# Performance work log

Hardware: AMD Instinct MI355X
Metric: run time of the kernel (lower is better)

The kernel has to match this reference:

```python
import jax, jax.numpy as jnp
import numpy as np
from jax import lax

B, T, E, H, A, V = 128, 64, 512, 512, 512, 10000


def setup_inputs() -> dict:
    key = jax.random.key(0)
    ks = jax.random.split(key, 16)
    # lengths: descending, in [1, T], first forced to T (pack_padded_sequence requirement)
    ln = np.asarray(jax.random.randint(ks[0], (B,), 1, T + 1))
    ln = np.sort(ln)[::-1].copy()
    ln[0] = T
    u = lambda k, s, a=0.1: jax.random.uniform(k, s, jnp.float32, -a, a)
    return {
        "features": jax.random.normal(ks[1], (B, E), jnp.float32),
        "captions": jax.random.randint(ks[2], (B, T - 1), 0, V),
        "lengths": jnp.asarray(ln, jnp.int64) if jax.config.jax_enable_x64 else jnp.asarray(ln, jnp.int32),
        "cnn_features": jax.random.normal(ks[3], (B, A), jnp.float32),
        "emb_W": u(ks[4], (V, E)),
        "W_ih": u(ks[5], (4 * H, E), 1.0 / np.sqrt(H)),
        "W_hh": u(ks[6], (4 * H, H), 1.0 / np.sqrt(H)),
        "b_ih": u(ks[7], (4 * H,), 1.0 / np.sqrt(H)),
        "b_hh": u(ks[8], (4 * H,), 1.0 / np.sqrt(H)),
        "att_W": u(ks[9], (A, H + E)),
        "att_b": jnp.zeros((A,), jnp.float32),
        "attd_W": u(ks[10], (E, A + E)),
        "attd_b": jnp.zeros((E,), jnp.float32),
        "out_W": u(ks[11], (V, H)),
        "out_b": jnp.zeros((V,), jnp.float32),
    }


def _lstm_cell(x, h, c, W_ih, W_hh, b_ih, b_hh):
    g = x @ W_ih.T + b_ih + h @ W_hh.T + b_hh  # (B, 4H)
    i, f, gg, o = jnp.split(g, 4, axis=-1)
    i = jax.nn.sigmoid(i); f = jax.nn.sigmoid(f)
    gg = jnp.tanh(gg); o = jax.nn.sigmoid(o)
    c2 = f * c + i * gg
    return o * jnp.tanh(c2), c2


def reference(features, captions, lengths, cnn_features, emb_W, W_ih, W_hh, b_ih, b_hh,
              att_W, att_b, attd_W, attd_b, out_W, out_b):
    emb = emb_W[captions]                                    # (B, T-1, E)
    xs = jnp.concatenate([features[:, None, :], emb], 1)     # (B, T, E)
    h0 = jnp.zeros((B, H), xs.dtype)
    c0 = jnp.zeros((B, H), xs.dtype)
    # step 0: plain LSTM on raw input, zero initial state (all sequences active)
    h1, c1 = _lstm_cell(xs[:, 0], h0, c0, W_ih, W_hh, b_ih, b_hh)

    def step(carry, inp):
        h, c = carry
        x, t = inp                                           # x: (B, E)
        aw = jax.nn.softmax(jnp.concatenate([x, h], 1) @ att_W.T + att_b, axis=1)
        attended = cnn_features * aw                         # (B, A)
        x2 = jnp.concatenate([x, attended], 1) @ attd_W.T + attd_b  # (B, E)
        h2, c2 = _lstm_cell(x2, h, c, W_ih, W_hh, b_ih, b_hh)
        active = (t < lengths)[:, None]
        h = jnp.where(active, h2, h)
        c = jnp.where(active, c2, c)
        return (h, c), jnp.where(active, h2, jnp.zeros_like(h2))

    xs_t = jnp.swapaxes(xs[:, 1:], 0, 1)                     # (T-1, B, E)
    _, outs = lax.scan(step, (h1, c1), (xs_t, jnp.arange(1, T)))
    hidden = jnp.concatenate([h1[None], outs], 0)            # (T, B, H)
    logits = hidden @ out_W.T + out_b                        # (T, B, V)
    valid = (jnp.arange(T)[:, None] < lengths[None, :])      # (T, B)
    return jnp.where(valid[:, :, None], logits, jnp.zeros_like(logits))
```

## Files before the change

kernel.cpp:

```cpp
#include <hip/hip_runtime.h>
#include <hip/hip_bf16.h>

#define B 128
#define T 64
#define E 512
#define H 512
#define AA 512
#define V 10000

typedef __hip_bfloat16 bf16;
typedef unsigned long long u64;
typedef unsigned short u16;
typedef __attribute__((ext_vector_type(8))) short bf16x8s;
typedef __attribute__((ext_vector_type(4))) float f32x4;

#define MFMA __builtin_amdgcn_mfma_f32_16x16x32_bf16

__device__ __forceinline__ bf16x8s ld8(const bf16* p) {
  return *reinterpret_cast<const bf16x8s*>(p);
}
__device__ __forceinline__ float sigm(float x) { return 1.f / (1.f + __expf(-x)); }
__device__ __forceinline__ float bf2f(u16 u) {
  return __uint_as_float(((unsigned)u) << 16);
}


__global__ __launch_bounds__(256) void kxs(const float* __restrict__ feat,
                                           const int* __restrict__ cap,
                                           const float* __restrict__ embW,
                                           bf16* __restrict__ xs) {
  int idx = blockIdx.x * 256 + threadIdx.x;
  int e4 = (idx & 127) << 2;
  int b = (idx >> 7) & 127;
  int t = idx >> 14;
  const float* src = (t == 0) ? (feat + (size_t)b * E)
                              : (embW + (size_t)cap[b * (T - 1) + (t - 1)] * E);
  float4 v = *reinterpret_cast<const float4*>(src + e4);
  bf16* d = xs + ((size_t)t * B + b) * E + e4;
  d[0] = __float2bfloat16(v.x); d[1] = __float2bfloat16(v.y);
  d[2] = __float2bfloat16(v.z); d[3] = __float2bfloat16(v.w);
}

__global__ __launch_bounds__(256) void kcast(const float* __restrict__ s,
                                             bf16* __restrict__ d, int n4) {
  int i = blockIdx.x * 256 + threadIdx.x;
  if (i >= n4) return;
  float4 v = *reinterpret_cast<const float4*>(s + (size_t)i * 4);
  d[i * 4 + 0] = __float2bfloat16(v.x); d[i * 4 + 1] = __float2bfloat16(v.y);
  d[i * 4 + 2] = __float2bfloat16(v.z); d[i * 4 + 3] = __float2bfloat16(v.w);
}

__global__ __launch_bounds__(256) void kslice(const float* __restrict__ src,
                                              bf16* __restrict__ dst, int c0) {
  int i = blockIdx.x * 256 + threadIdx.x;
  int row = i >> 7, c4 = (i & 127) << 2;
  float4 v = *reinterpret_cast<const float4*>(src + (size_t)row * 1024 + c0 + c4);
  bf16* d = dst + (size_t)row * 512 + c4;
  d[0] = __float2bfloat16(v.x); d[1] = __float2bfloat16(v.y);
  d[2] = __float2bfloat16(v.z); d[3] = __float2bfloat16(v.w);
}

__global__ __launch_bounds__(256) void ktrans(const float* __restrict__ src,
                                              bf16* __restrict__ dst, int coff) {
  __shared__ float tl[32][33];
  int bx = blockIdx.x & 15, by = blockIdx.x >> 4;
  int tx = threadIdx.x & 31, ty = threadIdx.x >> 5;
  for (int yy = ty; yy < 32; yy += 8)
    tl[yy][tx] = src[(size_t)(by * 32 + yy) * 1024 + coff + bx * 32 + tx];
  __syncthreads();
  for (int yy = ty; yy < 32; yy += 8)
    dst[(size_t)(bx * 32 + yy) * 512 + by * 32 + tx] = __float2bfloat16(tl[tx][yy]);
}

__global__ __launch_bounds__(256) void kpadW(const float* __restrict__ s,
                                             bf16* __restrict__ d) {
  int i = blockIdx.x * 256 + threadIdx.x;
  int row = (i << 2) / H;
  float4 v = make_float4(0.f, 0.f, 0.f, 0.f);
  if (row < V) v = *reinterpret_cast<const float4*>(s + (size_t)i * 4);
  d[i * 4 + 0] = __float2bfloat16(v.x); d[i * 4 + 1] = __float2bfloat16(v.y);
  d[i * 4 + 2] = __float2bfloat16(v.z); d[i * 4 + 3] = __float2bfloat16(v.w);
}

__global__ __launch_bounds__(256) void kgb(const float* __restrict__ bih,
                                           const float* __restrict__ bhh,
                                           const float* __restrict__ Wih_f,
                                           const float* __restrict__ attdb,
                                           float* __restrict__ gb0,
                                           float* __restrict__ gbA) {
  int g = blockIdx.x * 256 + threadIdx.x;
  if (g >= 2048) return;
  float b0 = bih[g] + bhh[g];
  float s = 0.f;
  for (int e = 0; e < 512; ++e) s += Wih_f[(size_t)g * 512 + e] * attdb[e];
  gb0[g] = b0; gbA[g] = b0 + s;
}

__global__ __launch_bounds__(256) void kgemm(const bf16* __restrict__ Ag,
                                             const bf16* __restrict__ Bg,
                                             const float* __restrict__ bias,
                                             bf16* __restrict__ outB,
                                             int nbn, int Nld) {
  __shared__ __align__(16) char lds[2][2][16384];
  const int nwg = gridDim.x;
  const int bid0 = blockIdx.x;
  const int wg = (bid0 & 7) * (nwg >> 3) + (bid0 >> 3);
  const int bm = wg / nbn, bn = wg % nbn;
  const int tid = threadIdx.x, w = tid >> 6, lane = tid & 63;
  const int fr = lane & 15, fq = lane >> 4, ko = fq << 3;
  const int mh = w >> 1, nh = w & 1;
  const bf16* Abase = Ag + (size_t)bm * 128 * 512;
  const bf16* Bbase = Bg + (size_t)bn * 128 * 512;
  f32x4 acc[4][4] = {};
  auto STAGE = [&](int buf, int k0) {
    #pragma unroll
    for (int m = 0; m < 2; ++m) {
      const bf16* base = m ? Bbase : Abase;
      #pragma unroll
      for (int it = 0; it < 4; ++it) {
        int si = tid + it * 256;
        int row = si >> 3;
        int s = (si & 7) ^ (row & 7);
        __builtin_amdgcn_global_load_lds(
          (const __attribute__((address_space(1))) void*)(base + (size_t)row * 512 + k0 + s * 8),
          (__attribute__((address_space(3))) void*)(&lds[buf][m][((tid & ~63) + it * 256) * 16]),
          16, 0, 0);
      }
    }
  };
  STAGE(0, 0);
  __syncthreads();
  for (int kt = 0; kt < 8; ++kt) {
    int cur = kt & 1;
    if (kt < 7) STAGE(cur ^ 1, (kt + 1) * 64);
    #pragma unroll
    for (int kk = 0; kk < 64; kk += 32) {
      bf16x8s a[4], b[4];
      #pragma unroll
      for (int i = 0; i < 4; ++i) {
        int ra = mh * 64 + i * 16 + fr;
        a[i] = *reinterpret_cast<const bf16x8s*>(
            &lds[cur][0][ra * 128 + ((((kk + ko) >> 3) ^ (ra & 7)) << 4)]);
        int rb = nh * 64 + i * 16 + fr;
        b[i] = *reinterpret_cast<const bf16x8s*>(
            &lds[cur][1][rb * 128 + ((((kk + ko) >> 3) ^ (rb & 7)) << 4)]);
      }
      #pragma unroll
      for (int mi = 0; mi < 4; ++mi)
        #pragma unroll
        for (int ni = 0; ni < 4; ++ni)
          acc[mi][ni] = MFMA(a[mi], b[ni], acc[mi][ni], 0, 0, 0);
    }
    __syncthreads();
  }
  #pragma unroll
  for (int mi = 0; mi < 4; ++mi)
    #pragma unroll
    for (int ni = 0; ni < 4; ++ni)
      #pragma unroll
      for (int j = 0; j < 4; ++j) {
        int row = bm * 128 + mh * 64 + mi * 16 + fq * 4 + j;
        int col = bn * 128 + nh * 64 + ni * 16 + fr;
        float bv = bias ? bias[col] : 0.f;
        outB[(size_t)row * Nld + col] = __float2bfloat16(acc[mi][ni][j] + bv);
      }
}

__global__ __launch_bounds__(256, 4) void kfinal(const bf16* __restrict__ Ag,
                                                 const bf16* __restrict__ Bg,
                                                 const float* __restrict__ bias,
                                                 const int* __restrict__ len,
                                                 float* __restrict__ out) {
  __shared__ __align__(16) char lds[2][2][8192];
  const int nwg = gridDim.x;
  const int bid0 = blockIdx.x;
  const int wg = (bid0 & 7) * (nwg >> 3) + (bid0 >> 3);
  const int bm = wg / 79, bn = wg % 79;
  const int tid = threadIdx.x, w = tid >> 6, lane = tid & 63;
  const int fr = lane & 15, fq = lane >> 4;
  const int mh = w >> 1, nh = w & 1;
  const bf16* Abase = Ag + (size_t)bm * 128 * 512;
  const bf16* Bbase = Bg + (size_t)bn * 128 * 512;
  f32x4 acc[4][4] = {};
  auto STAGE = [&](int buf, int k0) {
    #pragma unroll
    for (int m = 0; m < 2; ++m) {
      const bf16* base = m ? Bbase : Abase;
      #pragma unroll
      for (int it = 0; it < 2; ++it) {
        int u = it * 256 + tid;
        int row = u >> 2, c = u & 3;
        int cs = c ^ ((row >> 1) & 3);
        __builtin_amdgcn_global_load_lds(
          (const __attribute__((address_space(1))) void*)(base + (size_t)row * 512 + k0 + cs * 8),
          (__attribute__((address_space(3))) void*)(&lds[buf][m][((tid & ~63) + it * 256) * 16]),
          16, 0, 0);
      }
    }
  };
  STAGE(0, 0);
  __syncthreads();
  for (int kt = 0; kt < 16; ++kt) {
    int cur = kt & 1;
    if (kt < 15) STAGE(cur ^ 1, (kt + 1) * 32);
    bf16x8s a[4], b[4];
    #pragma unroll
    for (int i = 0; i < 4; ++i) {
      int ra = mh * 64 + i * 16 + fr;
      a[i] = *reinterpret_cast<const bf16x8s*>(
          &lds[cur][0][ra * 64 + ((fq ^ ((ra >> 1) & 3)) << 4)]);
      int rb = nh * 64 + i * 16 + fr;
      b[i] = *reinterpret_cast<const bf16x8s*>(
          &lds[cur][1][rb * 64 + ((fq ^ ((rb >> 1) & 3)) << 4)]);
    }
    #pragma unroll
    for (int mi = 0; mi < 4; ++mi)
      #pragma unroll
      for (int ni = 0; ni < 4; ++ni)
        acc[mi][ni] = MFMA(a[mi], b[ni], acc[mi][ni], 0, 0, 0);
    __syncthreads();
  }
  #pragma unroll
  for (int mi = 0; mi < 4; ++mi)
    #pragma unroll
    for (int ni = 0; ni < 4; ++ni)
      #pragma unroll
      for (int j = 0; j < 4; ++j) {
        int row = bm * 128 + mh * 64 + mi * 16 + fq * 4 + j;
        int col = bn * 128 + nh * 64 + ni * 16 + fr;
        if (col < V) {
          int tt = row >> 7, bb = row & 127;
          out[(size_t)row * V + col] = (tt < len[bb]) ? acc[mi][ni][j] + bias[col] : 0.f;
        }
      }
}

__global__ __launch_bounds__(512, 1) void kloop(
    const bf16* __restrict__ Sxb,
    const bf16* __restrict__ Gx,
    const bf16* __restrict__ Kc,
    const bf16* __restrict__ Whh,
    const bf16* __restrict__ WaH,
    const float* __restrict__ gb0,
    const float* __restrict__ gbA,
    const float* __restrict__ cnn,
    const int* __restrict__ len,
    bf16* __restrict__ hstore,
    bf16* __restrict__ pstore,
    float* __restrict__ Zbuf,
    bf16* __restrict__ hid,
    int* ticket, int* winner, int* flags) {
  __shared__ __align__(16) char KcS[65536];
  __shared__ __align__(16) char WhS[65536];
  __shared__ int steam[2];

  if (threadIdx.x == 0) {
    int xcc;
    asm volatile("s_getreg_b32 %0, hwreg(HW_REG_XCC_ID)" : "=s"(xcc));
    xcc &= 15;
    int my = __hip_atomic_fetch_add(&ticket[xcc], 1, __ATOMIC_RELAXED,
                                    __HIP_MEMORY_SCOPE_AGENT);
    if (my == 31) {
      int exp = -1;
      __hip_atomic_compare_exchange_strong(winner, &exp, xcc, __ATOMIC_RELAXED,
                                           __ATOMIC_RELAXED, __HIP_MEMORY_SCOPE_AGENT);
    }
    int wv;
    while ((wv = __hip_atomic_load(winner, __ATOMIC_RELAXED,
                                   __HIP_MEMORY_SCOPE_AGENT)) < 0)
      __builtin_amdgcn_s_sleep(8);
    steam[0] = (wv == xcc && my < 32) ? 1 : 0;
    steam[1] = my;
  }
  __syncthreads();
  if (!steam[0]) return;
  const int wid = steam[1];

  const int tid = threadIdx.x, w = tid >> 6, lane = tid & 63;
  const int fr = lane & 15, fq = lane >> 4, ko = fq << 3;
  const int cb = wid << 4;
  const int col = cb + fr;

  for (int u = tid; u < 4096; u += 512) {
    int row = u >> 6, chunk = u & 63;
    int g = (row >> 4) * 512 + cb + (row & 15);
    int off = row * 1024 + ((chunk ^ (row & 7)) << 4);
    *reinterpret_cast<bf16x8s*>(&KcS[off]) = ld8(Kc + (size_t)g * 512 + chunk * 8);
    *reinterpret_cast<bf16x8s*>(&WhS[off]) = ld8(Whh + (size_t)g * 512 + chunk * 8);
  }

  const int r0 = w * 16 + fq * 4;
  int4 lv4 = *reinterpret_cast<const int4*>(len + r0);
  int lv[4] = {lv4.x, lv4.y, lv4.z, lv4.w};
  float cnnv[4], gb0v[4], gbAv[4];
  #pragma unroll
  for (int j = 0; j < 4; ++j) cnnv[j] = cnn[(size_t)(r0 + j) * AA + col];
  #pragma unroll
  for (int q = 0; q < 4; ++q) {
    gb0v[q] = gb0[q * 512 + col];
    gbAv[q] = gbA[q * 512 + col];
  }
  float cstv[4] = {0.f, 0.f, 0.f, 0.f};
  u16 hpv[4] = {0, 0, 0, 0};
  __syncthreads();

  auto arrive = [&](int ep2) {
    __syncthreads();
    if (tid == 0)
      __hip_atomic_store(flags + wid * 16, ep2, __ATOMIC_RELAXED,
                         __HIP_MEMORY_SCOPE_AGENT);
  };
  auto wait = [&](int ep2) {
    if (tid < 64) {
      const int* fp = flags + (tid & 31) * 16;
      while (__ballot(__hip_atomic_load(fp, __ATOMIC_RELAXED,
                                        __HIP_MEMORY_SCOPE_AGENT) < ep2))
        __builtin_amdgcn_s_sleep(1);
    }
    __syncthreads();
  };

  int ep = 0;
  for (int t = 0; t < T; ++t) {
    if (t) { ++ep; arrive(ep); }
    u16 gxv[16];
    u16 sxv[4] = {0, 0, 0, 0};
    #pragma unroll
    for (int q = 0; q < 4; ++q)
      #pragma unroll
      for (int j = 0; j < 4; ++j)
        gxv[q * 4 + j] = __builtin_nontemporal_load(
            (const u16*)Gx + ((size_t)t * B + r0 + j) * 2048 + q * 512 + col);
    if (t) {
      #pragma unroll
      for (int j = 0; j < 4; ++j)
        sxv[j] = __builtin_nontemporal_load(
            (const u16*)Sxb + ((size_t)t * B + r0 + j) * AA + col);
    }
    const bf16* hin = hstore + (size_t)(t ? t - 1 : 0) * B * H;
    bf16* pst = pstore + (size_t)t * B * AA;
    if (t) {
      wait(ep);
      f32x4 acc1 = {};
      {
        const bf16* ha = hin + (size_t)(w * 16 + fr) * H + ko;
        const bf16* wb = WaH + (size_t)col * H + ko;
        #pragma unroll 4
        for (int k = 0; k < 512; k += 32)
          acc1 = MFMA(ld8(ha + k), ld8(wb + k), acc1, 0, 0, 0);
      }
      float pj[4];
      #pragma unroll
      for (int j = 0; j < 4; ++j) {
        pj[j] = __expf(acc1[j] + bf2f(sxv[j]));
        bf16 pb = __float2bfloat16(pj[j] * cnnv[j]);
        pst[(size_t)(r0 + j) * AA + col] = pb;
      }
      #pragma unroll
      for (int j = 0; j < 4; ++j) {
        float z = pj[j];
        z += __shfl_xor(z, 1); z += __shfl_xor(z, 2);
        z += __shfl_xor(z, 4); z += __shfl_xor(z, 8);
        if (fr == 0)
          __hip_atomic_fetch_add(Zbuf + t * B + r0 + j, z, __ATOMIC_RELAXED,
                                 __HIP_MEMORY_SCOPE_WORKGROUP);
      }
      ++ep; arrive(ep);
    }
    f32x4 accH[4] = {}, accP[4] = {};
    if (t) {
      {
        const bf16* ha = hin + (size_t)(w * 16 + fr) * H + ko;
        #pragma unroll 2
        for (int k = 0; k < 512; k += 32) {
          bf16x8s a = ld8(ha + k);
          #pragma unroll
          for (int q = 0; q < 4; ++q) {
            bf16x8s b = *reinterpret_cast<const bf16x8s*>(
                &WhS[(q * 16 + fr) * 1024 + ((((k >> 3) + fq) ^ (fr & 7)) << 4)]);
            accH[q] = MFMA(a, b, accH[q], 0, 0, 0);
          }
        }
      }
      wait(ep);
      {
        const bf16* pa = pst + (size_t)(w * 16 + fr) * AA + ko;
        #pragma unroll 2
        for (int k = 0; k < 512; k += 32) {
          bf16x8s a = ld8(pa + k);
          #pragma unroll
          for (int q = 0; q < 4; ++q) {
            bf16x8s b = *reinterpret_cast<const bf16x8s*>(
                &KcS[(q * 16 + fr) * 1024 + ((((k >> 3) + fq) ^ (fr & 7)) << 4)]);
            accP[q] = MFMA(a, b, accP[q], 0, 0, 0);
          }
        }
      }
      float4 zv = *reinterpret_cast<const float4*>(Zbuf + t * B + r0);
      float zp[4] = {zv.x, zv.y, zv.z, zv.w};
      #pragma unroll
      for (int q = 0; q < 4; ++q)
        #pragma unroll
        for (int j = 0; j < 4; ++j)
          accP[q][j] *= __fdividef(1.f, zp[j]);
    }
    float gsel[4];
    #pragma unroll
    for (int q = 0; q < 4; ++q) gsel[q] = t ? gbAv[q] : gb0v[q];
    #pragma unroll
    for (int j = 0; j < 4; ++j) {
      float gi = sigm(accP[0][j] + accH[0][j] + gsel[0] + bf2f(gxv[0 + j]));
      float gf = sigm(accP[1][j] + accH[1][j] + gsel[1] + bf2f(gxv[4 + j]));
      float gg = tanhf(accP[2][j] + accH[2][j] + gsel[2] + bf2f(gxv[8 + j]));
      float go = sigm(accP[3][j] + accH[3][j] + gsel[3] + bf2f(gxv[12 + j]));
      float c2 = gf * cstv[j] + gi * gg;
      float h2 = go * tanhf(c2);
      bool act = t < lv[j];
      if (act) cstv[j] = c2;
      bf16 hb = __float2bfloat16(h2);
      u16 hbits = *reinterpret_cast<u16*>(&hb);
      hpv[j] = act ? hbits : hpv[j];
      ((u16*)hstore)[((size_t)t * B + r0 + j) * H + col] = hpv[j];
      __builtin_nontemporal_store(act ? hbits : (u16)0,
          (u16*)hid + ((size_t)t * B + r0 + j) * H + col);
    }
  }
}


extern "C" void kernel_launch(void* const* d_in, const int* in_sizes, int n_in,
                              void* d_out, int out_size, void* d_ws, size_t ws_size,
                              hipStream_t stream) {
  const float* feat   = (const float*)d_in[0];
  const int*   cap    = (const int*)d_in[1];
  const int*   len    = (const int*)d_in[2];
  const float* cnn    = (const float*)d_in[3];
  const float* embW   = (const float*)d_in[4];
  const float* Wih_f  = (const float*)d_in[5];
  const float* Whh_f  = (const float*)d_in[6];
  const float* bih    = (const float*)d_in[7];
  const float* bhh    = (const float*)d_in[8];
  const float* attW_f = (const float*)d_in[9];
  const float* attb   = (const float*)d_in[10];
  const float* attdW_f= (const float*)d_in[11];
  const float* attdb  = (const float*)d_in[12];
  const float* outW_f = (const float*)d_in[13];
  const float* outb   = (const float*)d_in[14];
  float* out = (float*)d_out;
  char* ws = (char*)d_ws;

  size_t off = 0;
  auto alloc = [&](size_t n) { char* p = ws + off; off += (n + 255) & ~(size_t)255; return p; };
  bf16*  xs    = (bf16*)alloc(8388608);
  bf16*  WaX   = (bf16*)alloc(524288);
  bf16*  WaH   = (bf16*)alloc(524288);
  bf16*  WdXT  = (bf16*)alloc(524288);
  bf16*  WdAT  = (bf16*)alloc(524288);
  bf16*  Wihb  = (bf16*)alloc(2097152);
  bf16*  Whhb  = (bf16*)alloc(2097152);
  bf16*  Kc    = (bf16*)alloc(2097152);
  bf16*  outWp = (bf16*)alloc(10354688);
  bf16*  Sxb   = (bf16*)alloc(8388608);
  bf16*  Gx    = (bf16*)alloc(33554432);
  bf16*  hid   = (bf16*)alloc(8388608);
  bf16*  hstore= (bf16*)alloc(8388608);
  bf16*  pstore= (bf16*)alloc(8388608);
  float* gb0   = (float*)alloc(8192);
  float* gbA   = (float*)alloc(8192);
  float* Zbuf  = (float*)alloc(32768);
  int*   ticket= (int*)alloc(256);
  int*   winner= (int*)alloc(256);
  int*   flags = (int*)alloc(2048);
  bf16*  Kx    = pstore;

  kxs<<<4096, 256, 0, stream>>>(feat, cap, embW, xs);
  kslice<<<256, 256, 0, stream>>>(attW_f, WaX, 0);
  kslice<<<256, 256, 0, stream>>>(attW_f, WaH, 512);
  ktrans<<<256, 256, 0, stream>>>(attdW_f, WdXT, 0);
  ktrans<<<256, 256, 0, stream>>>(attdW_f, WdAT, 512);
  kcast<<<1024, 256, 0, stream>>>(Wih_f, Wihb, 262144);
  kcast<<<1024, 256, 0, stream>>>(Whh_f, Whhb, 262144);
  kpadW<<<5056, 256, 0, stream>>>(outW_f, outWp);
  kgb<<<8, 256, 0, stream>>>(bih, bhh, Wih_f, attdb, gb0, gbA);

  kgemm<<<256, 256, 0, stream>>>(xs, WaX, attb, Sxb, 4, 512);
  kgemm<<<64, 256, 0, stream>>>(Wihb, WdXT, nullptr, Kx, 4, 512);
  kgemm<<<64, 256, 0, stream>>>(Wihb, WdAT, nullptr, Kc, 4, 512);
  kgemm<<<1024, 256, 0, stream>>>(xs, Kx, nullptr, Gx, 16, 2048);
  kgemm<<<16, 256, 0, stream>>>(xs, Wihb, nullptr, Gx, 16, 2048);

  hipMemsetAsync(ticket, 0, 256, stream);
  hipMemsetAsync(winner, 0xFF, 256, stream);
  hipMemsetAsync(flags, 0, 2048, stream);
  hipMemsetAsync(Zbuf, 0, 32768, stream);

  kloop<<<256, 512, 0, stream>>>(Sxb, Gx, Kc, Whhb, WaH, gb0, gbA, cnn, len,
                                 hstore, pstore, Zbuf, hid, ticket, winner, flags);

  kfinal<<<5056, 256, 0, stream>>>(hid, outWp, outb, len, out);
}
```

Measured before the change: 1.706 ms.

## Prepack per-thread Gx/Sx inputs, stage WaH in LDS, reuse h fragments

A new kpack kernel rearranges the precomputed input-gate and attention-score tensors so each thread of the recurrent loop fetches its 16+4 values with a few contiguous 64-bit loads instead of scattered 2-byte loads. The recurrent kernel also caches its WaH slice in shared memory and loads the previous hidden state fragments once into registers, reusing them for both the attention and recurrent MFMAs. The goal is to shorten the serial per-step latency of the persistent loop, at the cost of an extra pass over about 40 MB and more register pressure.

Result: slower. 1.780 ms (+4.3%).

```diff
diff --git a/kernel.cpp b/kernel.cpp
--- a/kernel.cpp
+++ b/kernel.cpp
@@ -94,6 +94,33 @@
   float s = 0.f;
   for (int e = 0; e < 512; ++e) s += Wih_f[(size_t)g * 512 + e] * attdb[e];
   gb0[g] = b0; gbA[g] = b0 + s;
+}
+
+__global__ __launch_bounds__(512) void kpack(const u16* __restrict__ Gx,
+                                             const u16* __restrict__ Sxb,
+                                             u16* __restrict__ Gxp,
+                                             u16* __restrict__ Sxp) {
+  int bid = blockIdx.x;
+  int t = bid >> 5, wid = bid & 31;
+  int tid = threadIdx.x;
+  int w = tid >> 6, lane = tid & 63;
+  int fr = lane & 15, fq = lane >> 4;
+  int r0 = w * 16 + fq * 4;
+  int cb = wid << 4;
+  u16 g[16], s[4];
+  #pragma unroll
+  for (int q = 0; q < 4; ++q)
+    #pragma unroll
+    for (int j = 0; j < 4; ++j)
+      g[q * 4 + j] = Gx[((size_t)t * B + r0 + j) * 2048 + q * 512 + cb + fr];
+  #pragma unroll
+  for (int j = 0; j < 4; ++j)
+    s[j] = Sxb[((size_t)t * B + r0 + j) * AA + cb + fr];
+  size_t ob = ((size_t)bid * 512 + tid);
+  #pragma unroll
+  for (int k = 0; k < 16; ++k) Gxp[ob * 16 + k] = g[k];
+  #pragma unroll
+  for (int j = 0; j < 4; ++j) Sxp[ob * 4 + j] = s[j];
 }
 
 __global__ __launch_bounds__(256) void kgemm(const bf16* __restrict__ Ag,
@@ -236,8 +263,8 @@
 }
 
 __global__ __launch_bounds__(512, 1) void kloop(
-    const bf16* __restrict__ Sxb,
-    const bf16* __restrict__ Gx,
+    const u16* __restrict__ Sxp,
+    const u16* __restrict__ Gxp,
     const bf16* __restrict__ Kc,
     const bf16* __restrict__ Whh,
     const bf16* __restrict__ WaH,
@@ -252,6 +279,7 @@
     int* ticket, int* winner, int* flags) {
   __shared__ __align__(16) char KcS[65536];
   __shared__ __align__(16) char WhS[65536];
+  __shared__ __align__(16) char WaS[16384];
   __shared__ int steam[2];
 
   if (threadIdx.x == 0) {
@@ -287,6 +315,11 @@
     int off = row * 1024 + ((chunk ^ (row & 7)) << 4);
     *reinterpret_cast<bf16x8s*>(&KcS[off]) = ld8(Kc + (size_t)g * 512 + chunk * 8);
     *reinterpret_cast<bf16x8s*>(&WhS[off]) = ld8(Whh + (size_t)g * 512 + chunk * 8);
+  }
+  for (int u = tid; u < 1024; u += 512) {
+    int row = u >> 6, chunk = u & 63;
+    *reinterpret_cast<bf16x8s*>(&WaS[row * 1024 + ((chunk ^ (row & 7)) << 4)]) =
+        ld8(WaH + (size_t)(cb + row) * 512 + chunk * 8);
   }
 
   const int r0 = w * 16 + fq * 4;
@@ -323,38 +356,37 @@
   int ep = 0;
   for (int t = 0; t < T; ++t) {
     if (t) { ++ep; arrive(ep); }
-    u16 gxv[16];
-    u16 sxv[4] = {0, 0, 0, 0};
-    #pragma unroll
-    for (int q = 0; q < 4; ++q)
-      #pragma unroll
-      for (int j = 0; j < 4; ++j)
-        gxv[q * 4 + j] = __builtin_nontemporal_load(
-            (const u16*)Gx + ((size_t)t * B + r0 + j) * 2048 + q * 512 + col);
-    if (t) {
-      #pragma unroll
-      for (int j = 0; j < 4; ++j)
-        sxv[j] = __builtin_nontemporal_load(
-            (const u16*)Sxb + ((size_t)t * B + r0 + j) * AA + col);
-    }
+    size_t pb = ((size_t)(t * 32 + wid) * 512 + tid);
+    u64 gw[4];
+    const u64* gp = reinterpret_cast<const u64*>(Gxp) + pb * 4;
+    #pragma unroll
+    for (int k = 0; k < 4; ++k) gw[k] = __builtin_nontemporal_load(gp + k);
+    u64 sw = 0;
+    if (t) sw = __builtin_nontemporal_load(reinterpret_cast<const u64*>(Sxp) + pb);
     const bf16* hin = hstore + (size_t)(t ? t - 1 : 0) * B * H;
     bf16* pst = pstore + (size_t)t * B * AA;
+    f32x4 accH[4] = {}, accP[4] = {};
     if (t) {
       wait(ep);
-      f32x4 acc1 = {};
+      bf16x8s a_h[16];
       {
         const bf16* ha = hin + (size_t)(w * 16 + fr) * H + ko;
-        const bf16* wb = WaH + (size_t)col * H + ko;
-        #pragma unroll 4
-        for (int k = 0; k < 512; k += 32)
-          acc1 = MFMA(ld8(ha + k), ld8(wb + k), acc1, 0, 0, 0);
+        #pragma unroll
+        for (int i = 0; i < 16; ++i) a_h[i] = ld8(ha + i * 32);
+      }
+      f32x4 acc1 = {};
+      #pragma unroll
+      for (int k = 0; k < 512; k += 32) {
+        bf16x8s b = *reinterpret_cast<const bf16x8s*>(
+            &WaS[fr * 1024 + ((((k >> 3) + fq) ^ (fr & 7)) << 4)]);
+        acc1 = MFMA(a_h[k >> 5], b, acc1, 0, 0, 0);
       }
       float pj[4];
       #pragma unroll
       for (int j = 0; j < 4; ++j) {
-        pj[j] = __expf(acc1[j] + bf2f(sxv[j]));
-        bf16 pb = __float2bfloat16(pj[j] * cnnv[j]);
-        pst[(size_t)(r0 + j) * AA + col] = pb;
+        pj[j] = __expf(acc1[j] + bf2f((u16)(sw >> (16 * j))));
+        bf16 pb2 = __float2bfloat16(pj[j] * cnnv[j]);
+        pst[(size_t)(r0 + j) * AA + col] = pb2;
       }
       #pragma unroll
       for (int j = 0; j < 4; ++j) {
@@ -366,20 +398,14 @@
                                  __HIP_MEMORY_SCOPE_WORKGROUP);
       }
       ++ep; arrive(ep);
-    }
-    f32x4 accH[4] = {}, accP[4] = {};
-    if (t) {
-      {
-        const bf16* ha = hin + (size_t)(w * 16 + fr) * H + ko;
-        #pragma unroll 2
-        for (int k = 0; k < 512; k += 32) {
-          bf16x8s a = ld8(ha + k);
-          #pragma unroll
-          for (int q = 0; q < 4; ++q) {
-            bf16x8s b = *reinterpret_cast<const bf16x8s*>(
-                &WhS[(q * 16 + fr) * 1024 + ((((k >> 3) + fq) ^ (fr & 7)) << 4)]);
-            accH[q] = MFMA(a, b, accH[q], 0, 0, 0);
-          }
+      #pragma unroll 2
+      for (int k = 0; k < 512; k += 32) {
+        bf16x8s a = a_h[k >> 5];
+        #pragma unroll
+        for (int q = 0; q < 4; ++q) {
+          bf16x8s b = *reinterpret_cast<const bf16x8s*>(
+              &WhS[(q * 16 + fr) * 1024 + ((((k >> 3) + fq) ^ (fr & 7)) << 4)]);
+          accH[q] = MFMA(a, b, accH[q], 0, 0, 0);
         }
       }
       wait(ep);
@@ -409,10 +435,10 @@
     for (int q = 0; q < 4; ++q) gsel[q] = t ? gbAv[q] : gb0v[q];
     #pragma unroll
     for (int j = 0; j < 4; ++j) {
-      float gi = sigm(accP[0][j] + accH[0][j] + gsel[0] + bf2f(gxv[0 + j]));
-      float gf = sigm(accP[1][j] + accH[1][j] + gsel[1] + bf2f(gxv[4 + j]));
-      float gg = tanhf(accP[2][j] + accH[2][j] + gsel[2] + bf2f(gxv[8 + j]));
-      float go = sigm(accP[3][j] + accH[3][j] + gsel[3] + bf2f(gxv[12 + j]));
+      float gi = sigm(accP[0][j] + accH[0][j] + gsel[0] + bf2f((u16)(gw[0] >> (16 * j))));
+      float gf = sigm(accP[1][j] + accH[1][j] + gsel[1] + bf2f((u16)(gw[1] >> (16 * j))));
+      float gg = tanhf(accP[2][j] + accH[2][j] + gsel[2] + bf2f((u16)(gw[2] >> (16 * j))));
+      float go = sigm(accP[3][j] + accH[3][j] + gsel[3] + bf2f((u16)(gw[3] >> (16 * j))));
       float c2 = gf * cstv[j] + gi * gg;
       float h2 = go * tanhf(c2);
       bool act = t < lv[j];
@@ -421,8 +447,7 @@
       u16 hbits = *reinterpret_cast<u16*>(&hb);
       hpv[j] = act ? hbits : hpv[j];
       ((u16*)hstore)[((size_t)t * B + r0 + j) * H + col] = hpv[j];
-      __builtin_nontemporal_store(act ? hbits : (u16)0,
-          (u16*)hid + ((size_t)t * B + r0 + j) * H + col);
+      ((u16*)hid)[((size_t)t * B + r0 + j) * H + col] = act ? hbits : (u16)0;
     }
   }
 }
@@ -462,6 +487,8 @@
   bf16*  outWp = (bf16*)alloc(10354688);
   bf16*  Sxb   = (bf16*)alloc(8388608);
   bf16*  Gx    = (bf16*)alloc(33554432);
+  u16*   Gxp   = (u16*)alloc(33554432);
+  u16*   Sxp   = (u16*)alloc(8388608);
   bf16*  hid   = (bf16*)alloc(8388608);
   bf16*  hstore= (bf16*)alloc(8388608);
   bf16*  pstore= (bf16*)alloc(8388608);
@@ -489,12 +516,14 @@
   kgemm<<<1024, 256, 0, stream>>>(xs, Kx, nullptr, Gx, 16, 2048);
   kgemm<<<16, 256, 0, stream>>>(xs, Wihb, nullptr, Gx, 16, 2048);
 
+  kpack<<<2048, 512, 0, stream>>>((const u16*)Gx, (const u16*)Sxb, Gxp, Sxp);
+
   hipMemsetAsync(ticket, 0, 256, stream);
   hipMemsetAsync(winner, 0xFF, 256, stream);
   hipMemsetAsync(flags, 0, 2048, stream);
   hipMemsetAsync(Zbuf, 0, 32768, stream);
 
-  kloop<<<256, 512, 0, stream>>>(Sxb, Gx, Kc, Whhb, WaH, gb0, gbA, cnn, len,
+  kloop<<<256, 512, 0, stream>>>(Sxp, Gxp, Kc, Whhb, WaH, gb0, gbA, cnn, len,
                                  hstore, pstore, Zbuf, hid, ticket, winner, flags);
 
   kfinal<<<5056, 256, 0, stream>>>(hid, outWp, outb, len, out);
```

## Double wavefronts in recurrent loop, split gate work, prepack per-step inputs

Applied to the files above, without the earlier changes.

The persistent recurrent kernel now runs 1024 threads per block instead of 512. Waves are split into two halves: one computes the attention-score MFMA and the softmax numerator, while the other starts the hidden-state gate MFMAs in parallel. Gate pre-activations are gathered through shared memory so each thread finishes the LSTM update for two rows. A new packing kernel rearranges the precomputed input-gate and attention inputs into a per-block contiguous layout, so each thread can fetch its values with wide coalesced loads. The cost is an extra pass over roughly 40MB, more shared memory, and an extra block-wide barrier every step.

New measurement: 2.106 ms. 1.23x slower.

```diff
diff --git a/kernel.cpp b/kernel.cpp
--- a/kernel.cpp
+++ b/kernel.cpp
@@ -1,5 +1,6 @@
 #include <hip/hip_runtime.h>
 #include <hip/hip_bf16.h>
+#include <limits.h>
 
 #define B 128
 #define T 64
@@ -94,6 +95,37 @@
   float s = 0.f;
   for (int e = 0; e < 512; ++e) s += Wih_f[(size_t)g * 512 + e] * attdb[e];
   gb0[g] = b0; gbA[g] = b0 + s;
+}
+
+__global__ __launch_bounds__(1024) void kpack(const u16* __restrict__ Gx,
+                                              const u16* __restrict__ Sxb,
+                                              u16* __restrict__ Gxp,
+                                              u16* __restrict__ Sxp) {
+  int bid = blockIdx.x;
+  int t = bid >> 5, wid = bid & 31;
+  int cb = wid << 4;
+  int tid = threadIdx.x;
+  {
+    int ccol = tid & 15, rp = tid >> 4;
+    u16 g[8];
+    #pragma unroll
+    for (int q = 0; q < 4; ++q)
+      #pragma unroll
+      for (int j = 0; j < 2; ++j)
+        g[q * 2 + j] = Gx[((size_t)t * B + 2 * rp + j) * 2048 + q * 512 + cb + ccol];
+    u16* dst = Gxp + ((size_t)bid * 1024 + tid) * 8;
+    #pragma unroll
+    for (int k = 0; k < 8; ++k) dst[k] = g[k];
+  }
+  if (((tid >> 6) & 1) == 0) {
+    int rt = tid >> 7, lane = tid & 63;
+    int fr = lane & 15, fq = lane >> 4;
+    int p = rt * 64 + lane;
+    #pragma unroll
+    for (int j = 0; j < 4; ++j)
+      Sxp[((size_t)bid * 512 + p) * 4 + j] =
+          Sxb[((size_t)t * B + rt * 16 + fq * 4 + j) * AA + cb + fr];
+  }
 }
 
 __global__ __launch_bounds__(256) void kgemm(const bf16* __restrict__ Ag,
@@ -235,9 +267,9 @@
       }
 }
 
-__global__ __launch_bounds__(512, 1) void kloop(
-    const bf16* __restrict__ Sxb,
-    const bf16* __restrict__ Gx,
+__global__ __launch_bounds__(1024, 1) void kloop(
+    const u16* __restrict__ Sxp,
+    const u16* __restrict__ Gxp,
     const bf16* __restrict__ Kc,
     const bf16* __restrict__ Whh,
     const bf16* __restrict__ WaH,
@@ -250,9 +282,10 @@
     float* __restrict__ Zbuf,
     bf16* __restrict__ hid,
     int* ticket, int* winner, int* flags) {
+  __shared__ __align__(16) char WhS[65536];
   __shared__ __align__(16) char KcS[65536];
-  __shared__ __align__(16) char WhS[65536];
-  __shared__ int steam[2];
+  __shared__ __align__(16) float gateX[4][128][16];
+  int* steam = reinterpret_cast<int*>(&gateX[0][0][0]);
 
   if (threadIdx.x == 0) {
     int xcc;
@@ -265,43 +298,47 @@
       __hip_atomic_compare_exchange_strong(winner, &exp, xcc, __ATOMIC_RELAXED,
                                            __ATOMIC_RELAXED, __HIP_MEMORY_SCOPE_AGENT);
     }
-    int wv;
-    while ((wv = __hip_atomic_load(winner, __ATOMIC_RELAXED,
-                                   __HIP_MEMORY_SCOPE_AGENT)) < 0)
+    int wv2;
+    while ((wv2 = __hip_atomic_load(winner, __ATOMIC_RELAXED,
+                                    __HIP_MEMORY_SCOPE_AGENT)) < 0)
       __builtin_amdgcn_s_sleep(8);
-    steam[0] = (wv == xcc && my < 32) ? 1 : 0;
+    steam[0] = (wv2 == xcc && my < 32) ? 1 : 0;
     steam[1] = my;
   }
   __syncthreads();
   if (!steam[0]) return;
   const int wid = steam[1];
 
-  const int tid = threadIdx.x, w = tid >> 6, lane = tid & 63;
+  const int tid = threadIdx.x, wv = tid >> 6, lane = tid & 63;
   const int fr = lane & 15, fq = lane >> 4, ko = fq << 3;
-  const int cb = wid << 4;
-  const int col = cb + fr;
-
-  for (int u = tid; u < 4096; u += 512) {
+  const int rt = wv >> 1, gh = wv & 1;
+  const int cb = wid << 4, col = cb + fr;
+  const int r0 = rt * 16 + fq * 4;
+  const int arow = rt * 16 + fr;
+  const int ccol = tid & 15, crp = tid >> 4;
+
+  for (int u = tid; u < 4096; u += 1024) {
     int row = u >> 6, chunk = u & 63;
     int g = (row >> 4) * 512 + cb + (row & 15);
     int off = row * 1024 + ((chunk ^ (row & 7)) << 4);
+    *reinterpret_cast<bf16x8s*>(&WhS[off]) = ld8(Whh + (size_t)g * 512 + chunk * 8);
     *reinterpret_cast<bf16x8s*>(&KcS[off]) = ld8(Kc + (size_t)g * 512 + chunk * 8);
-    *reinterpret_cast<bf16x8s*>(&WhS[off]) = ld8(Whh + (size_t)g * 512 + chunk * 8);
-  }
-
-  const int r0 = w * 16 + fq * 4;
-  int4 lv4 = *reinterpret_cast<const int4*>(len + r0);
-  int lv[4] = {lv4.x, lv4.y, lv4.z, lv4.w};
-  float cnnv[4], gb0v[4], gbAv[4];
-  #pragma unroll
-  for (int j = 0; j < 4; ++j) cnnv[j] = cnn[(size_t)(r0 + j) * AA + col];
+  }
+  float cnnv[4] = {0.f, 0.f, 0.f, 0.f};
+  if (gh == 0) {
+    #pragma unroll
+    for (int j = 0; j < 4; ++j) cnnv[j] = cnn[(size_t)(r0 + j) * AA + col];
+  }
+  int2 lv2 = *reinterpret_cast<const int2*>(len + 2 * crp);
+  float gb0v[4], gbAv[4];
   #pragma unroll
   for (int q = 0; q < 4; ++q) {
-    gb0v[q] = gb0[q * 512 + col];
-    gbAv[q] = gbA[q * 512 + col];
-  }
-  float cstv[4] = {0.f, 0.f, 0.f, 0.f};
-  u16 hpv[4] = {0, 0, 0, 0};
+    gb0v[q] = gb0[q * 512 + cb + ccol];
+    gbAv[q] = gbA[q * 512 + cb + ccol];
+  }
+  float cstv[2] = {0.f, 0.f};
+  u16 hpv[2] = {0, 0};
+  const bf16* WaB = WaH + (size_t)col * 512;
   __syncthreads();
 
   auto arrive = [&](int ep2) {
@@ -323,106 +360,114 @@
   int ep = 0;
   for (int t = 0; t < T; ++t) {
     if (t) { ++ep; arrive(ep); }
-    u16 gxv[16];
-    u16 sxv[4] = {0, 0, 0, 0};
-    #pragma unroll
-    for (int q = 0; q < 4; ++q)
-      #pragma unroll
-      for (int j = 0; j < 4; ++j)
-        gxv[q * 4 + j] = __builtin_nontemporal_load(
-            (const u16*)Gx + ((size_t)t * B + r0 + j) * 2048 + q * 512 + col);
-    if (t) {
-      #pragma unroll
-      for (int j = 0; j < 4; ++j)
-        sxv[j] = __builtin_nontemporal_load(
-            (const u16*)Sxb + ((size_t)t * B + r0 + j) * AA + col);
-    }
+    const u64* gp = reinterpret_cast<const u64*>(Gxp) +
+                    ((size_t)(t * 32 + wid) * 1024 + tid) * 2;
+    u64 g01 = __builtin_nontemporal_load(gp);
+    u64 g23 = __builtin_nontemporal_load(gp + 1);
+    u64 sw = 0;
+    if (t && gh == 0)
+      sw = __builtin_nontemporal_load(reinterpret_cast<const u64*>(Sxp) +
+                                      (size_t)(t * 32 + wid) * 512 + rt * 64 + lane);
     const bf16* hin = hstore + (size_t)(t ? t - 1 : 0) * B * H;
     bf16* pst = pstore + (size_t)t * B * AA;
+    f32x4 accH[2] = {}, accP[2] = {};
     if (t) {
       wait(ep);
-      f32x4 acc1 = {};
-      {
-        const bf16* ha = hin + (size_t)(w * 16 + fr) * H + ko;
-        const bf16* wb = WaH + (size_t)col * H + ko;
+      const bf16* ha = hin + (size_t)arow * H + ko;
+      if (gh == 0) {
+        f32x4 acc1 = {};
         #pragma unroll 4
         for (int k = 0; k < 512; k += 32)
-          acc1 = MFMA(ld8(ha + k), ld8(wb + k), acc1, 0, 0, 0);
-      }
-      float pj[4];
-      #pragma unroll
-      for (int j = 0; j < 4; ++j) {
-        pj[j] = __expf(acc1[j] + bf2f(sxv[j]));
-        bf16 pb = __float2bfloat16(pj[j] * cnnv[j]);
-        pst[(size_t)(r0 + j) * AA + col] = pb;
-      }
-      #pragma unroll
-      for (int j = 0; j < 4; ++j) {
-        float z = pj[j];
-        z += __shfl_xor(z, 1); z += __shfl_xor(z, 2);
-        z += __shfl_xor(z, 4); z += __shfl_xor(z, 8);
-        if (fr == 0)
-          __hip_atomic_fetch_add(Zbuf + t * B + r0 + j, z, __ATOMIC_RELAXED,
-                                 __HIP_MEMORY_SCOPE_WORKGROUP);
-      }
-      ++ep; arrive(ep);
-    }
-    f32x4 accH[4] = {}, accP[4] = {};
-    if (t) {
-      {
-        const bf16* ha = hin + (size_t)(w * 16 + fr) * H + ko;
+          acc1 = MFMA(ld8(ha + k), ld8(WaB + k + ko), acc1, 0, 0, 0);
+        float pj[4];
+        #pragma unroll
+        for (int j = 0; j < 4; ++j) {
+          pj[j] = __expf(acc1[j] + bf2f((u16)(sw >> (16 * j))));
+          bf16 pb2 = __float2bfloat16(pj[j] * cnnv[j]);
+          ((u16*)pst)[(size_t)(r0 + j) * AA + col] = *reinterpret_cast<u16*>(&pb2);
+        }
+        #pragma unroll
+        for (int j = 0; j < 4; ++j) {
+          float z = pj[j];
+          z += __shfl_xor(z, 1); z += __shfl_xor(z, 2);
+          z += __shfl_xor(z, 4); z += __shfl_xor(z, 8);
+          if (fr == 0)
+            __hip_atomic_fetch_add(Zbuf + t * B + r0 + j, z, __ATOMIC_RELAXED,
+                                   __HIP_MEMORY_SCOPE_WORKGROUP);
+        }
+      } else {
         #pragma unroll 2
         for (int k = 0; k < 512; k += 32) {
           bf16x8s a = ld8(ha + k);
           #pragma unroll
-          for (int q = 0; q < 4; ++q) {
+          for (int qi = 0; qi < 2; ++qi) {
             bf16x8s b = *reinterpret_cast<const bf16x8s*>(
-                &WhS[(q * 16 + fr) * 1024 + ((((k >> 3) + fq) ^ (fr & 7)) << 4)]);
-            accH[q] = MFMA(a, b, accH[q], 0, 0, 0);
+                &WhS[((2 + qi) * 16 + fr) * 1024 + ((((k >> 3) + fq) ^ (fr & 7)) << 4)]);
+            accH[qi] = MFMA(a, b, accH[qi], 0, 0, 0);
           }
         }
       }
-      wait(ep);
-      {
-        const bf16* pa = pst + (size_t)(w * 16 + fr) * AA + ko;
+      ++ep; arrive(ep);
+      if (gh == 0) {
         #pragma unroll 2
         for (int k = 0; k < 512; k += 32) {
-          bf16x8s a = ld8(pa + k);
+          bf16x8s a = ld8(ha + k);
           #pragma unroll
-          for (int q = 0; q < 4; ++q) {
+          for (int qi = 0; qi < 2; ++qi) {
             bf16x8s b = *reinterpret_cast<const bf16x8s*>(
-                &KcS[(q * 16 + fr) * 1024 + ((((k >> 3) + fq) ^ (fr & 7)) << 4)]);
-            accP[q] = MFMA(a, b, accP[q], 0, 0, 0);
+                &WhS[(qi * 16 + fr) * 1024 + ((((k >> 3) + fq) ^ (fr & 7)) << 4)]);
+            accH[qi] = MFMA(a, b, accH[qi], 0, 0, 0);
           }
         }
       }
+      wait(ep);
+      const bf16* pa = pst + (size_t)arow * AA + ko;
+      #pragma unroll 2
+      for (int k = 0; k < 512; k += 32) {
+        bf16x8s a = ld8(pa + k);
+        #pragma unroll
+        for (int qi = 0; qi < 2; ++qi) {
+          bf16x8s b = *reinterpret_cast<const bf16x8s*>(
+              &KcS[((gh * 2 + qi) * 16 + fr) * 1024 + ((((k >> 3) + fq) ^ (fr & 7)) << 4)]);
+          accP[qi] = MFMA(a, b, accP[qi], 0, 0, 0);
+        }
+      }
       float4 zv = *reinterpret_cast<const float4*>(Zbuf + t * B + r0);
       float zp[4] = {zv.x, zv.y, zv.z, zv.w};
       #pragma unroll
-      for (int q = 0; q < 4; ++q)
+      for (int qi = 0; qi < 2; ++qi)
         #pragma unroll
         for (int j = 0; j < 4; ++j)
-          accP[q][j] *= __fdividef(1.f, zp[j]);
-    }
-    float gsel[4];
-    #pragma unroll
-    for (int q = 0; q < 4; ++q) gsel[q] = t ? gbAv[q] : gb0v[q];
-    #pragma unroll
-    for (int j = 0; j < 4; ++j) {
-      float gi = sigm(accP[0][j] + accH[0][j] + gsel[0] + bf2f(gxv[0 + j]));
-      float gf = sigm(accP[1][j] + accH[1][j] + gsel[1] + bf2f(gxv[4 + j]));
-      float gg = tanhf(accP[2][j] + accH[2][j] + gsel[2] + bf2f(gxv[8 + j]));
-      float go = sigm(accP[3][j] + accH[3][j] + gsel[3] + bf2f(gxv[12 + j]));
+          gateX[gh * 2 + qi][r0 + j][fr] =
+              accH[qi][j] + accP[qi][j] * __fdividef(1.f, zp[j]);
+    }
+    __syncthreads();
+    #pragma unroll
+    for (int j = 0; j < 2; ++j) {
+      int row = 2 * crp + j;
+      float z0 = 0.f, z1 = 0.f, z2 = 0.f, z3 = 0.f;
+      if (t) {
+        z0 = gateX[0][row][ccol]; z1 = gateX[1][row][ccol];
+        z2 = gateX[2][row][ccol]; z3 = gateX[3][row][ccol];
+      }
+      float b0 = t ? gbAv[0] : gb0v[0];
+      float b1 = t ? gbAv[1] : gb0v[1];
+      float b2 = t ? gbAv[2] : gb0v[2];
+      float b3 = t ? gbAv[3] : gb0v[3];
+      float gi = sigm(z0 + b0 + bf2f((u16)(g01 >> (16 * (0 + j)))));
+      float gf = sigm(z1 + b1 + bf2f((u16)(g01 >> (16 * (2 + j)))));
+      float gg = tanhf(z2 + b2 + bf2f((u16)(g23 >> (16 * (0 + j)))));
+      float go = sigm(z3 + b3 + bf2f((u16)(g23 >> (16 * (2 + j)))));
       float c2 = gf * cstv[j] + gi * gg;
       float h2 = go * tanhf(c2);
-      bool act = t < lv[j];
+      bool act = t < (j ? lv2.y : lv2.x);
       if (act) cstv[j] = c2;
       bf16 hb = __float2bfloat16(h2);
       u16 hbits = *reinterpret_cast<u16*>(&hb);
       hpv[j] = act ? hbits : hpv[j];
-      ((u16*)hstore)[((size_t)t * B + r0 + j) * H + col] = hpv[j];
+      ((u16*)hstore)[((size_t)t * B + row) * H + cb + ccol] = hpv[j];
       __builtin_nontemporal_store(act ? hbits : (u16)0,
-          (u16*)hid + ((size_t)t * B + r0 + j) * H + col);
+          (u16*)hid + ((size_t)t * B + row) * H + cb + ccol);
     }
   }
 }
@@ -462,6 +507,8 @@
   bf16*  outWp = (bf16*)alloc(10354688);
   bf16*  Sxb   = (bf16*)alloc(8388608);
   bf16*  Gx    = (bf16*)alloc(33554432);
+  u16*   Gxp   = (u16*)alloc(33554432);
+  u16*   Sxp   = (u16*)alloc(8388608);
   bf16*  hid   = (bf16*)alloc(8388608);
   bf16*  hstore= (bf16*)alloc(8388608);
   bf16*  pstore= (bf16*)alloc(8388608);
@@ -470,7 +517,7 @@
   float* Zbuf  = (float*)alloc(32768);
   int*   ticket= (int*)alloc(256);
   int*   winner= (int*)alloc(256);
-  int*   flags = (int*)alloc(2048);
+  int*   flags = (int*)alloc(4096);
   bf16*  Kx    = pstore;
 
   kxs<<<4096, 256, 0, stream>>>(feat, cap, embW, xs);
@@ -489,13 +536,15 @@
   kgemm<<<1024, 256, 0, stream>>>(xs, Kx, nullptr, Gx, 16, 2048);
   kgemm<<<16, 256, 0, stream>>>(xs, Wihb, nullptr, Gx, 16, 2048);
 
+  kpack<<<2048, 1024, 0, stream>>>((const u16*)Gx, (const u16*)Sxb, Gxp, Sxp);
+
   hipMemsetAsync(ticket, 0, 256, stream);
   hipMemsetAsync(winner, 0xFF, 256, stream);
-  hipMemsetAsync(flags, 0, 2048, stream);
+  hipMemsetAsync(flags, 0, 4096, stream);
   hipMemsetAsync(Zbuf, 0, 32768, stream);
 
-  kloop<<<256, 512, 0, stream>>>(Sxb, Gx, Kc, Whhb, WaH, gb0, gbA, cnn, len,
-                                 hstore, pstore, Zbuf, hid, ticket, winner, flags);
+  kloop<<<256, 1024, 0, stream>>>(Sxp, Gxp, Kc, Whhb, WaH, gb0, gbA, cnn, len,
+                                  hstore, pstore, Zbuf, hid, ticket, winner, flags);
 
   kfinal<<<5056, 256, 0, stream>>>(hid, outWp, outb, len, out);
 }
```
